# Kernel tuning notes

Measured on AMD Instinct MI355X. Metric: run time of the kernel, lower is better.

The kernel has to match this reference:

```python
import jax, jax.numpy as jnp
import numpy as np

D_MODEL = 1024
N_HEADS = 16
HEAD = D_MODEL // N_HEADS
SEQ_THRESHOLD = 2048
EPS = 1e-12  # torch F.normalize eps


def setup_inputs() -> dict:
    key = jax.random.key(0)
    ks = jax.random.split(key, 12)
    B, L = 2, 2048
    s = 1.0 / np.sqrt(D_MODEL)
    inp = {
        "query": jax.random.normal(ks[0], (B, L, D_MODEL), jnp.float32),
        "key": jax.random.normal(ks[1], (B, L, D_MODEL), jnp.float32),
        "value": jax.random.normal(ks[2], (B, L, D_MODEL), jnp.float32),
        "mask": jnp.ones((B, 1, 1, L), jnp.int32),
        "Wq": jax.random.normal(ks[3], (D_MODEL, D_MODEL), jnp.float32) * s,
        "bq": jnp.zeros((D_MODEL,), jnp.float32),
        "Wk": jax.random.normal(ks[4], (D_MODEL, D_MODEL), jnp.float32) * s,
        "bk": jnp.zeros((D_MODEL,), jnp.float32),
        "Wv": jax.random.normal(ks[5], (D_MODEL, D_MODEL), jnp.float32) * s,
        "bv": jnp.zeros((D_MODEL,), jnp.float32),
        "Wo": jax.random.normal(ks[6], (D_MODEL, D_MODEL), jnp.float32) * s,
        "bo": jnp.zeros((D_MODEL,), jnp.float32),
        "scale": jnp.asarray(np.log2(SEQ_THRESHOLD**2 - SEQ_THRESHOLD), jnp.float32),
    }
    return inp


def _split_heads(x):  # [B,L,D] -> [B,H,L,hd]
    B, L, _ = x.shape
    return x.reshape(B, L, N_HEADS, HEAD).transpose(0, 2, 1, 3)


def _l2norm(x):
    n = jnp.sqrt(jnp.sum(x * x, axis=-1, keepdims=True))
    return x / jnp.maximum(n, EPS)


def reference(query, key, value, mask, Wq, bq, Wk, bk, Wv, bv, Wo, bo, scale):
    Q = _split_heads(query @ Wq.T + bq)
    K = _split_heads(key @ Wk.T + bk)
    V = _split_heads(value @ Wv.T + bv)
    Q = _l2norm(Q)
    K = _l2norm(K)
    # scaled cosine attention scores [B,H,Lq,Lk]
    scores = scale * jnp.einsum("bhqd,bhkd->bhqk", Q, K)
    scores = jnp.where(mask == 0, jnp.float32(-1e18), scores)
    attn = jax.nn.softmax(scores, axis=-1)
    ctx = jnp.einsum("bhqk,bhkd->bhqd", attn, V)
    B, H, Lq, hd = ctx.shape
    ctx = ctx.transpose(0, 2, 1, 3).reshape(B, Lq, H * hd)
    out = ctx @ Wo.T + bo
    return (out, attn)
```

## Files before the change

### kernel.cpp

```cpp
#include <hip/hip_runtime.h>
#include <hip/hip_bf16.h>
#include <stdint.h>

typedef __attribute__((ext_vector_type(8))) short bf16x8;
typedef __attribute__((ext_vector_type(4))) float f32x4;

#define LSEQ 2048
#define DM 1024
#define NH 16
#define HD 64

__device__ __forceinline__ unsigned short bf16r(float f) {
  unsigned u = __builtin_bit_cast(unsigned, f);
  u = (u + 0x7FFFu + ((u >> 16) & 1u)) >> 16;
  return (unsigned short)u;
}
__device__ __forceinline__ float bf16f(unsigned short h) {
  unsigned u = ((unsigned)h) << 16;
  return __builtin_bit_cast(float, u);
}
__device__ __forceinline__ unsigned cvt_pk_bf16(float a, float b) {
  unsigned r;
  asm("v_cvt_pk_bf16_f32 %0, %1, %2" : "=v"(r) : "v"(a), "v"(b));
  return r;
}

__device__ __forceinline__ void async16(const void* g, void* l) {
  __builtin_amdgcn_global_load_lds(
      (const __attribute__((address_space(1))) unsigned int*)g,
      (__attribute__((address_space(3))) unsigned int*)l, 16, 0, 0);
}

__device__ __forceinline__ bf16x8 lds_frag_swz(const unsigned short* base, int row, int colbyte) {
  int addr = row * 128 + colbyte;
  addr ^= ((row & 7) << 4);
  return *(const bf16x8*)((const char*)base + addr);
}
__device__ __forceinline__ bf16x8 lds_frag_swzV(const unsigned short* base, int row, int colbyte) {
  int addr = row * 256 + colbyte;
  addr ^= ((row & 15) << 4);
  return *(const bf16x8*)((const char*)base + addr);
}

__global__ __launch_bounds__(256) void cvt3(const float* __restrict__ s0,
                                            const float* __restrict__ s1,
                                            const float* __restrict__ s2,
                                            unsigned short* __restrict__ d0,
                                            unsigned short* __restrict__ d1,
                                            unsigned short* __restrict__ d2, int n8) {
  int y = blockIdx.y;
  const float* s = (y == 0) ? s0 : (y == 1) ? s1 : s2;
  unsigned short* d = (y == 0) ? d0 : (y == 1) ? d1 : d2;
  int i = blockIdx.x * 256 + threadIdx.x;
  if (i >= n8) return;
  const float4* sp = (const float4*)s;
  float4 a = sp[2 * i], b = sp[2 * i + 1];
  union { unsigned short u[8]; uint4 v; } r;
  r.u[0] = bf16r(a.x); r.u[1] = bf16r(a.y); r.u[2] = bf16r(a.z); r.u[3] = bf16r(a.w);
  r.u[4] = bf16r(b.x); r.u[5] = bf16r(b.y); r.u[6] = bf16r(b.z); r.u[7] = bf16r(b.w);
  ((uint4*)d)[i] = r.v;
}
__global__ __launch_bounds__(256) void cvt4(const float* __restrict__ s0,
                                            const float* __restrict__ s1,
                                            const float* __restrict__ s2,
                                            const float* __restrict__ s3,
                                            unsigned short* __restrict__ d0,
                                            unsigned short* __restrict__ d1,
                                            unsigned short* __restrict__ d2,
                                            unsigned short* __restrict__ d3, int n8) {
  int y = blockIdx.y;
  const float* s = (y == 0) ? s0 : (y == 1) ? s1 : (y == 2) ? s2 : s3;
  unsigned short* d = (y == 0) ? d0 : (y == 1) ? d1 : (y == 2) ? d2 : d3;
  int i = blockIdx.x * 256 + threadIdx.x;
  if (i >= n8) return;
  const float4* sp = (const float4*)s;
  float4 a = sp[2 * i], b = sp[2 * i + 1];
  union { unsigned short u[8]; uint4 v; } r;
  r.u[0] = bf16r(a.x); r.u[1] = bf16r(a.y); r.u[2] = bf16r(a.z); r.u[3] = bf16r(a.w);
  r.u[4] = bf16r(b.x); r.u[5] = bf16r(b.y); r.u[6] = bf16r(b.z); r.u[7] = bf16r(b.w);
  ((uint4*)d)[i] = r.v;
}

template <int MODE>
__device__ __forceinline__ void gemm_core(const unsigned short* __restrict__ A,
                                          const unsigned short* __restrict__ Bw,
                                          const float* __restrict__ bias,
                                          void* __restrict__ Cout,
                                          unsigned short* As, unsigned short* Bs) {
  const int t = threadIdx.x, lane = t & 63, wid = t >> 6;
  const int mt = blockIdx.x, nt = blockIdx.y;
  const int wm = (wid >> 1) * 64, wn = (wid & 1) * 64;
  const int lq = lane >> 4, lr = lane & 15;

  f32x4 acc[4][4];
#pragma unroll
  for (int i = 0; i < 4; ++i)
#pragma unroll
    for (int j = 0; j < 4; ++j) acc[i][j] = (f32x4){0.f, 0.f, 0.f, 0.f};

  auto stage = [&](int k0) {
#pragma unroll
    for (int i = 0; i < 4; ++i) {
      int chunk = i * 256 + t;
      int row = chunk >> 3, j = chunk & 7;
      int sj = j ^ (row & 7);
      async16(A + (size_t)(mt * 128 + row) * DM + k0 + sj * 8, (char*)As + chunk * 16);
    }
#pragma unroll
    for (int i = 0; i < 4; ++i) {
      int chunk = i * 256 + t;
      int row = chunk >> 3, j = chunk & 7;
      int sj = j ^ (row & 7);
      async16(Bw + (size_t)(nt * 128 + row) * DM + k0 + sj * 8, (char*)Bs + chunk * 16);
    }
  };

  stage(0);
  for (int kt = 0; kt < DM / 64; ++kt) {
    __syncthreads();
    bf16x8 af[4][2], bfr[4][2];
#pragma unroll
    for (int mf = 0; mf < 4; ++mf) {
      int row = wm + mf * 16 + lr;
#pragma unroll
      for (int ks = 0; ks < 2; ++ks)
        af[mf][ks] = lds_frag_swz(As, row, ks * 64 + lq * 16);
    }
#pragma unroll
    for (int nf = 0; nf < 4; ++nf) {
      int row = wn + nf * 16 + lr;
#pragma unroll
      for (int ks = 0; ks < 2; ++ks)
        bfr[nf][ks] = lds_frag_swz(Bs, row, ks * 64 + lq * 16);
    }
    __syncthreads();
    if (kt + 1 < DM / 64) stage((kt + 1) * 64);
#pragma unroll
    for (int ks = 0; ks < 2; ++ks)
#pragma unroll
      for (int mf = 0; mf < 4; ++mf)
#pragma unroll
        for (int nf = 0; nf < 4; ++nf)
          acc[mf][nf] = __builtin_amdgcn_mfma_f32_16x16x32_bf16(af[mf][ks], bfr[nf][ks],
                                                                acc[mf][nf], 0, 0, 0);
  }

  const int gn0 = nt * 128 + wn;
  float bv[4];
#pragma unroll
  for (int nf = 0; nf < 4; ++nf) bv[nf] = bias[gn0 + nf * 16 + lr];
#pragma unroll
  for (int mf = 0; mf < 4; ++mf) {
    float v[4][4];
#pragma unroll
    for (int nf = 0; nf < 4; ++nf)
#pragma unroll
      for (int r = 0; r < 4; ++r) v[nf][r] = acc[mf][nf][r] + bv[nf];
    if (MODE == 1) {
#pragma unroll
      for (int r = 0; r < 4; ++r) {
        float ss = v[0][r] * v[0][r] + v[1][r] * v[1][r] + v[2][r] * v[2][r] + v[3][r] * v[3][r];
        ss += __shfl_xor(ss, 1, 64);
        ss += __shfl_xor(ss, 2, 64);
        ss += __shfl_xor(ss, 4, 64);
        ss += __shfl_xor(ss, 8, 64);
        float rn = 1.0f / fmaxf(sqrtf(ss), 1e-12f);
#pragma unroll
        for (int nf = 0; nf < 4; ++nf) v[nf][r] *= rn;
      }
    }
    const int gm0 = mt * 128 + wm + mf * 16 + lq * 4;
    if (MODE == 2) {
      float* C = (float*)Cout;
#pragma unroll
      for (int r = 0; r < 4; ++r)
#pragma unroll
        for (int nf = 0; nf < 4; ++nf)
          C[(size_t)(gm0 + r) * DM + gn0 + nf * 16 + lr] = v[nf][r];
    } else if (MODE == 3) {
      unsigned short* Vt = (unsigned short*)Cout;
      const int bb = gm0 >> 11, ll = gm0 & 2047;
#pragma unroll
      for (int nf = 0; nf < 4; ++nf) {
        int col = gn0 + nf * 16 + lr;
        int hh = col >> 6, dd = col & 63;
        ushort4 o;
        o.x = bf16r(v[nf][0]); o.y = bf16r(v[nf][1]);
        o.z = bf16r(v[nf][2]); o.w = bf16r(v[nf][3]);
        *(ushort4*)&Vt[(size_t)((bb * NH + hh) * HD + dd) * LSEQ + ll] = o;
      }
    } else {
      unsigned short* C = (unsigned short*)Cout;
#pragma unroll
      for (int r = 0; r < 4; ++r)
#pragma unroll
        for (int nf = 0; nf < 4; ++nf)
          C[(size_t)(gm0 + r) * DM + gn0 + nf * 16 + lr] = bf16r(v[nf][r]);
    }
  }
}

__global__ __launch_bounds__(256) void gemm_qkv(
    const unsigned short* __restrict__ A0, const unsigned short* __restrict__ A1,
    const unsigned short* __restrict__ A2, const unsigned short* __restrict__ W0,
    const unsigned short* __restrict__ W1, const unsigned short* __restrict__ W2,
    const float* __restrict__ b0, const float* __restrict__ b1, const float* __restrict__ b2,
    unsigned short* __restrict__ C0, unsigned short* __restrict__ C1,
    unsigned short* __restrict__ C2) {
  __shared__ unsigned short As[128 * 64];
  __shared__ unsigned short Bs[128 * 64];
  int z = blockIdx.z;
  if (z == 0) gemm_core<1>(A0, W0, b0, C0, As, Bs);
  else if (z == 1) gemm_core<1>(A1, W1, b1, C1, As, Bs);
  else gemm_core<3>(A2, W2, b2, C2, As, Bs);
}

__global__ __launch_bounds__(256) void gemm_o(const unsigned short* __restrict__ A,
                                              const unsigned short* __restrict__ W,
                                              const float* __restrict__ bias,
                                              float* __restrict__ C) {
  __shared__ unsigned short As[128 * 64];
  __shared__ unsigned short Bs[128 * 64];
  gemm_core<2>(A, W, bias, C, As, Bs);
}

__global__ __launch_bounds__(256, 4) void attn_kernel(
    const unsigned short* __restrict__ Qn, const unsigned short* __restrict__ Kn,
    const unsigned short* __restrict__ Vt, const int* __restrict__ mask,
    const float* __restrict__ scale_p, float* __restrict__ attn_out,
    unsigned short* __restrict__ ctx) {
  __shared__ unsigned short QVs[64 * 128];
  __shared__ unsigned short Ks[128 * 64];
  __shared__ unsigned short Ms[2048];
  const int qt = blockIdx.x, h = blockIdx.y, b = blockIdx.z;
  const int t = threadIdx.x, lane = t & 63, wid = t >> 6;
  const int lq = lane >> 4, lr = lane & 15;
  const int wq = wid * 16;
  const float k2 = scale_p[0] * 1.4426950408889634f;

  const unsigned short* Qg = Qn + ((size_t)(b * LSEQ + qt * 64) * DM + h * HD);
  const unsigned short* Kg = Kn + ((size_t)b * LSEQ * DM + h * HD);
  const unsigned short* Vg = Vt + (size_t)(b * NH + h) * HD * LSEQ;
  float* attn_g = attn_out + ((size_t)((b * NH + h) * LSEQ + qt * 64)) * LSEQ;
  const int* mg = mask + b * LSEQ;

  auto stageK = [&](int k0) {
#pragma unroll
    for (int i = 0; i < 4; ++i) {
      int chunk = i * 256 + t;
      int row = chunk >> 3, j = chunk & 7;
      async16(Kg + (size_t)(k0 + row) * DM + (j ^ (row & 7)) * 8, (char*)Ks + chunk * 16);
    }
  };
  auto stageV = [&](int k0) {
#pragma unroll
    for (int i = 0; i < 4; ++i) {
      int chunk = i * 256 + t;
      int row = chunk >> 4, j = chunk & 15;
      async16(Vg + (size_t)row * LSEQ + k0 + (j ^ (row & 15)) * 8, (char*)QVs + chunk * 16);
    }
  };

  {
    const int4* mp = (const int4*)mg;
    int4 m0 = mp[t * 2], m1 = mp[t * 2 + 1];
    union { unsigned short u[8]; uint4 v; } mo;
    mo.u[0] = m0.x ? 0x3F80 : 0; mo.u[1] = m0.y ? 0x3F80 : 0;
    mo.u[2] = m0.z ? 0x3F80 : 0; mo.u[3] = m0.w ? 0x3F80 : 0;
    mo.u[4] = m1.x ? 0x3F80 : 0; mo.u[5] = m1.y ? 0x3F80 : 0;
    mo.u[6] = m1.z ? 0x3F80 : 0; mo.u[7] = m1.w ? 0x3F80 : 0;
    ((uint4*)Ms)[t] = mo.v;
  }
#pragma unroll
  for (int i = 0; i < 2; ++i) {
    int chunk = i * 256 + t;
    int row = chunk >> 3, j = chunk & 7;
    async16(Qg + (size_t)row * DM + (j ^ (row & 7)) * 8, (char*)QVs + chunk * 16);
  }
  stageK(0);

  bf16x8 qa[2];
  float rsum = 0.f;

  for (int kt = 0; kt < LSEQ / 128; ++kt) {
    __syncthreads();
    if (kt == 0) {
      qa[0] = lds_frag_swz(QVs, wq + lr, lq * 16);
      qa[1] = lds_frag_swz(QVs, wq + lr, 64 + lq * 16);
    }
#pragma unroll
    for (int nf = 0; nf < 8; ++nf) {
      bf16x8 k0f = lds_frag_swz(Ks, nf * 16 + lr, lq * 16);
      bf16x8 k1f = lds_frag_swz(Ks, nf * 16 + lr, 64 + lq * 16);
      f32x4 z = (f32x4){0.f, 0.f, 0.f, 0.f};
      z = __builtin_amdgcn_mfma_f32_16x16x32_bf16(k0f, qa[0], z, 0, 0, 0);
      z = __builtin_amdgcn_mfma_f32_16x16x32_bf16(k1f, qa[1], z, 0, 0, 0);
      ushort4 m4 = *(const ushort4*)&Ms[kt * 128 + nf * 16 + lq * 4];
      rsum += exp2f(z[0] * k2) * bf16f(m4.x);
      rsum += exp2f(z[1] * k2) * bf16f(m4.y);
      rsum += exp2f(z[2] * k2) * bf16f(m4.z);
      rsum += exp2f(z[3] * k2) * bf16f(m4.w);
    }
    __syncthreads();
    if (kt + 1 < LSEQ / 128) stageK((kt + 1) * 128);
  }
  rsum += __shfl_xor(rsum, 16, 64);
  rsum += __shfl_xor(rsum, 32, 64);
  const float sinv = 1.0f / fmaxf(rsum, 1e-30f);

  stageK(0);
  stageV(0);
  f32x4 opv[4];
#pragma unroll
  for (int nf = 0; nf < 4; ++nf) opv[nf] = (f32x4){0.f, 0.f, 0.f, 0.f};
  const int s0 = (lq & 1) * 32 + lr, s1 = s0 + 16;
  const bool hi = (lq >> 1) != 0;

  for (int kt = 0; kt < LSEQ / 128; ++kt) {
    __syncthreads();
    unsigned pw[16];
#pragma unroll
    for (int nf = 0; nf < 8; ++nf) {
      bf16x8 k0f = lds_frag_swz(Ks, nf * 16 + lr, lq * 16);
      bf16x8 k1f = lds_frag_swz(Ks, nf * 16 + lr, 64 + lq * 16);
      f32x4 z = (f32x4){0.f, 0.f, 0.f, 0.f};
      z = __builtin_amdgcn_mfma_f32_16x16x32_bf16(k0f, qa[0], z, 0, 0, 0);
      z = __builtin_amdgcn_mfma_f32_16x16x32_bf16(k1f, qa[1], z, 0, 0, 0);
      ushort4 m4 = *(const ushort4*)&Ms[kt * 128 + nf * 16 + lq * 4];
      float p0 = exp2f(z[0] * k2) * bf16f(m4.x) * sinv;
      float p1 = exp2f(z[1] * k2) * bf16f(m4.y) * sinv;
      float p2 = exp2f(z[2] * k2) * bf16f(m4.z) * sinv;
      float p3 = exp2f(z[3] * k2) * bf16f(m4.w) * sinv;
      f32x4 st = (f32x4){p0, p1, p2, p3};
      __builtin_nontemporal_store(
          st, (f32x4*)(attn_g + (size_t)(wq + lr) * LSEQ + kt * 128 + nf * 16 + lq * 4));
      pw[nf * 2] = cvt_pk_bf16(p0, p1);
      pw[nf * 2 + 1] = cvt_pk_bf16(p2, p3);
    }
#pragma unroll
    for (int ks = 0; ks < 4; ++ks) {
      unsigned a0 = pw[4 * ks], a1 = pw[4 * ks + 1];
      unsigned b0 = pw[4 * ks + 2], b1 = pw[4 * ks + 3];
      unsigned ua0 = __shfl((int)a0, s0, 64), ua1 = __shfl((int)a1, s0, 64);
      unsigned ua2 = __shfl((int)a0, s1, 64), ua3 = __shfl((int)a1, s1, 64);
      unsigned ub0 = __shfl((int)b0, s0, 64), ub1 = __shfl((int)b1, s0, 64);
      unsigned ub2 = __shfl((int)b0, s1, 64), ub3 = __shfl((int)b1, s1, 64);
      union { unsigned w[4]; bf16x8 v; } pf;
      pf.w[0] = hi ? ub0 : ua0;
      pf.w[1] = hi ? ub1 : ua1;
      pf.w[2] = hi ? ub2 : ua2;
      pf.w[3] = hi ? ub3 : ua3;
#pragma unroll
      for (int nf = 0; nf < 4; ++nf) {
        bf16x8 vb = lds_frag_swzV(QVs, nf * 16 + lr, ks * 64 + lq * 16);
        opv[nf] = __builtin_amdgcn_mfma_f32_16x16x32_bf16(vb, pf.v, opv[nf], 0, 0, 0);
      }
    }
    __syncthreads();
    if (kt + 1 < LSEQ / 128) { stageK((kt + 1) * 128); stageV((kt + 1) * 128); }
  }
#pragma unroll
  for (int nf = 0; nf < 4; ++nf) {
    ushort4 o;
    o.x = bf16r(opv[nf][0]); o.y = bf16r(opv[nf][1]);
    o.z = bf16r(opv[nf][2]); o.w = bf16r(opv[nf][3]);
    *(ushort4*)&ctx[(size_t)(b * LSEQ + qt * 64 + wq + lr) * DM + h * HD + nf * 16 + lq * 4] = o;
  }
}

extern "C" void kernel_launch(void* const* d_in, const int* in_sizes, int n_in,
                              void* d_out, int out_size, void* d_ws, size_t ws_size,
                              hipStream_t stream) {
  const float* query = (const float*)d_in[0];
  const float* key_ = (const float*)d_in[1];
  const float* value = (const float*)d_in[2];
  const int* mask = (const int*)d_in[3];
  const float* Wq = (const float*)d_in[4];
  const float* bq = (const float*)d_in[5];
  const float* Wk = (const float*)d_in[6];
  const float* bk = (const float*)d_in[7];
  const float* Wv = (const float*)d_in[8];
  const float* bv = (const float*)d_in[9];
  const float* Wo = (const float*)d_in[10];
  const float* bo = (const float*)d_in[11];
  const float* scale = (const float*)d_in[12];

  char* ws = (char*)d_ws;
  const size_t XB = 8388608;
  const size_t WB = 2097152;
  unsigned short* qb = (unsigned short*)(ws);
  unsigned short* kb = (unsigned short*)(ws + XB);
  unsigned short* vb = (unsigned short*)(ws + 2 * XB);
  unsigned short* wqb = (unsigned short*)(ws + 3 * XB);
  unsigned short* wkb = (unsigned short*)(ws + 3 * XB + WB);
  unsigned short* wvb = (unsigned short*)(ws + 3 * XB + 2 * WB);
  unsigned short* wob = (unsigned short*)(ws + 3 * XB + 3 * WB);
  unsigned short* Qnb = (unsigned short*)(ws + 3 * XB + 4 * WB);
  unsigned short* Knb = (unsigned short*)(ws + 4 * XB + 4 * WB);
  unsigned short* Vtb = (unsigned short*)(ws + 5 * XB + 4 * WB);
  unsigned short* ctxb = (unsigned short*)(ws + 6 * XB + 4 * WB);

  cvt3<<<dim3(2048, 3), 256, 0, stream>>>(query, key_, value, qb, kb, vb, 524288);
  cvt4<<<dim3(512, 4), 256, 0, stream>>>(Wq, Wk, Wv, Wo, wqb, wkb, wvb, wob, 131072);

  gemm_qkv<<<dim3(32, 8, 3), 256, 0, stream>>>(qb, kb, vb, wqb, wkb, wvb, bq, bk, bv,
                                               Qnb, Knb, Vtb);

  float* attn_out = (float*)d_out + 4194304;
  attn_kernel<<<dim3(32, NH, 2), 256, 0, stream>>>(Qnb, Knb, Vtb, mask, scale, attn_out, ctxb);

  gemm_o<<<dim3(32, 8), 256, 0, stream>>>(ctxb, wob, bo, (float*)d_out);
}
```

Before: 287.9 us.

## Split attention warps 2x2 over query and key tiles, swizzle block order

Each warp now handles 32 query rows and half of each 128-key tile rather than 16 query rows and the full tile. Every K fragment loaded from LDS therefore feeds two query fragments, halving K fragment LDS reads per MFMA. Row sums and partial PV accumulators are combined across the two key-half warps through shared memory, which adds a sync and an LDS reduction at the end. The grid is flattened and swizzled so that consecutive blocks spread over heads and batches, and the exp2f calls become the hardware exp2 builtin.

```diff
diff --git a/kernel.cpp b/kernel.cpp
--- a/kernel.cpp
+++ b/kernel.cpp
@@ -232,10 +232,15 @@
   __shared__ unsigned short QVs[64 * 128];
   __shared__ unsigned short Ks[128 * 64];
   __shared__ unsigned short Ms[2048];
-  const int qt = blockIdx.x, h = blockIdx.y, b = blockIdx.z;
+  __shared__ float Rs[2][2][32];
+
+  const int raw = blockIdx.x;
+  const int swz = (raw & 7) * 128 + (raw >> 3);
+  const int qt = swz & 31, h = (swz >> 5) & 15, b = swz >> 9;
+
   const int t = threadIdx.x, lane = t & 63, wid = t >> 6;
   const int lq = lane >> 4, lr = lane & 15;
-  const int wq = wid * 16;
+  const int qg = wid >> 1, kg = wid & 1;
   const float k2 = scale_p[0] * 1.4426950408889634f;
 
   const unsigned short* Qg = Qn + ((size_t)(b * LSEQ + qt * 64) * DM + h * HD);
@@ -279,92 +284,152 @@
   }
   stageK(0);
 
-  bf16x8 qa[2];
-  float rsum = 0.f;
+  bf16x8 qb[2][2];
+  float rs[2] = {0.f, 0.f};
 
   for (int kt = 0; kt < LSEQ / 128; ++kt) {
     __syncthreads();
     if (kt == 0) {
-      qa[0] = lds_frag_swz(QVs, wq + lr, lq * 16);
-      qa[1] = lds_frag_swz(QVs, wq + lr, 64 + lq * 16);
-    }
-#pragma unroll
-    for (int nf = 0; nf < 8; ++nf) {
-      bf16x8 k0f = lds_frag_swz(Ks, nf * 16 + lr, lq * 16);
-      bf16x8 k1f = lds_frag_swz(Ks, nf * 16 + lr, 64 + lq * 16);
-      f32x4 z = (f32x4){0.f, 0.f, 0.f, 0.f};
-      z = __builtin_amdgcn_mfma_f32_16x16x32_bf16(k0f, qa[0], z, 0, 0, 0);
-      z = __builtin_amdgcn_mfma_f32_16x16x32_bf16(k1f, qa[1], z, 0, 0, 0);
-      ushort4 m4 = *(const ushort4*)&Ms[kt * 128 + nf * 16 + lq * 4];
-      rsum += exp2f(z[0] * k2) * bf16f(m4.x);
-      rsum += exp2f(z[1] * k2) * bf16f(m4.y);
-      rsum += exp2f(z[2] * k2) * bf16f(m4.z);
-      rsum += exp2f(z[3] * k2) * bf16f(m4.w);
+#pragma unroll
+      for (int qf = 0; qf < 2; ++qf)
+#pragma unroll
+        for (int dh = 0; dh < 2; ++dh)
+          qb[qf][dh] = lds_frag_swz(QVs, qg * 32 + qf * 16 + lr, dh * 64 + lq * 16);
+    }
+#pragma unroll
+    for (int kf = 0; kf < 4; ++kf) {
+      int krow = kg * 64 + kf * 16 + lr;
+      bf16x8 a0 = lds_frag_swz(Ks, krow, lq * 16);
+      bf16x8 a1 = lds_frag_swz(Ks, krow, 64 + lq * 16);
+      ushort4 m4 = *(const ushort4*)&Ms[kt * 128 + kg * 64 + kf * 16 + lq * 4];
+#pragma unroll
+      for (int qf = 0; qf < 2; ++qf) {
+        f32x4 z = (f32x4){0.f, 0.f, 0.f, 0.f};
+        z = __builtin_amdgcn_mfma_f32_16x16x32_bf16(a0, qb[qf][0], z, 0, 0, 0);
+        z = __builtin_amdgcn_mfma_f32_16x16x32_bf16(a1, qb[qf][1], z, 0, 0, 0);
+        rs[qf] += __builtin_amdgcn_exp2f(z[0] * k2) * bf16f(m4.x);
+        rs[qf] += __builtin_amdgcn_exp2f(z[1] * k2) * bf16f(m4.y);
+        rs[qf] += __builtin_amdgcn_exp2f(z[2] * k2) * bf16f(m4.z);
+        rs[qf] += __builtin_amdgcn_exp2f(z[3] * k2) * bf16f(m4.w);
+      }
     }
     __syncthreads();
     if (kt + 1 < LSEQ / 128) stageK((kt + 1) * 128);
   }
-  rsum += __shfl_xor(rsum, 16, 64);
-  rsum += __shfl_xor(rsum, 32, 64);
-  const float sinv = 1.0f / fmaxf(rsum, 1e-30f);
-
+#pragma unroll
+  for (int qf = 0; qf < 2; ++qf) {
+    rs[qf] += __shfl_xor(rs[qf], 16, 64);
+    rs[qf] += __shfl_xor(rs[qf], 32, 64);
+  }
+  if (lq == 0) {
+    Rs[qg][kg][lr] = rs[0];
+    Rs[qg][kg][16 + lr] = rs[1];
+  }
+  __syncthreads();
+  float sinv[2];
+#pragma unroll
+  for (int qf = 0; qf < 2; ++qf) {
+    float tot = Rs[qg][0][qf * 16 + lr] + Rs[qg][1][qf * 16 + lr];
+    sinv[qf] = 1.0f / fmaxf(tot, 1e-30f);
+  }
   stageK(0);
   stageV(0);
-  f32x4 opv[4];
-#pragma unroll
-  for (int nf = 0; nf < 4; ++nf) opv[nf] = (f32x4){0.f, 0.f, 0.f, 0.f};
-  const int s0 = (lq & 1) * 32 + lr, s1 = s0 + 16;
-  const bool hi = (lq >> 1) != 0;
+
+  f32x4 acc[4][2];
+#pragma unroll
+  for (int df = 0; df < 4; ++df)
+#pragma unroll
+    for (int qf = 0; qf < 2; ++qf) acc[df][qf] = (f32x4){0.f, 0.f, 0.f, 0.f};
+  const int sA = ((lane & 16) ? 32 : 0) + lr;
+  const int sB = sA + 16;
+  const bool selHi = (lane & 32) != 0;
 
   for (int kt = 0; kt < LSEQ / 128; ++kt) {
     __syncthreads();
-    unsigned pw[16];
-#pragma unroll
-    for (int nf = 0; nf < 8; ++nf) {
-      bf16x8 k0f = lds_frag_swz(Ks, nf * 16 + lr, lq * 16);
-      bf16x8 k1f = lds_frag_swz(Ks, nf * 16 + lr, 64 + lq * 16);
-      f32x4 z = (f32x4){0.f, 0.f, 0.f, 0.f};
-      z = __builtin_amdgcn_mfma_f32_16x16x32_bf16(k0f, qa[0], z, 0, 0, 0);
-      z = __builtin_amdgcn_mfma_f32_16x16x32_bf16(k1f, qa[1], z, 0, 0, 0);
-      ushort4 m4 = *(const ushort4*)&Ms[kt * 128 + nf * 16 + lq * 4];
-      float p0 = exp2f(z[0] * k2) * bf16f(m4.x) * sinv;
-      float p1 = exp2f(z[1] * k2) * bf16f(m4.y) * sinv;
-      float p2 = exp2f(z[2] * k2) * bf16f(m4.z) * sinv;
-      float p3 = exp2f(z[3] * k2) * bf16f(m4.w) * sinv;
-      f32x4 st = (f32x4){p0, p1, p2, p3};
-      __builtin_nontemporal_store(
-          st, (f32x4*)(attn_g + (size_t)(wq + lr) * LSEQ + kt * 128 + nf * 16 + lq * 4));
-      pw[nf * 2] = cvt_pk_bf16(p0, p1);
-      pw[nf * 2 + 1] = cvt_pk_bf16(p2, p3);
-    }
-#pragma unroll
-    for (int ks = 0; ks < 4; ++ks) {
-      unsigned a0 = pw[4 * ks], a1 = pw[4 * ks + 1];
-      unsigned b0 = pw[4 * ks + 2], b1 = pw[4 * ks + 3];
-      unsigned ua0 = __shfl((int)a0, s0, 64), ua1 = __shfl((int)a1, s0, 64);
-      unsigned ua2 = __shfl((int)a0, s1, 64), ua3 = __shfl((int)a1, s1, 64);
-      unsigned ub0 = __shfl((int)b0, s0, 64), ub1 = __shfl((int)b1, s0, 64);
-      unsigned ub2 = __shfl((int)b0, s1, 64), ub3 = __shfl((int)b1, s1, 64);
-      union { unsigned w[4]; bf16x8 v; } pf;
-      pf.w[0] = hi ? ub0 : ua0;
-      pf.w[1] = hi ? ub1 : ua1;
-      pf.w[2] = hi ? ub2 : ua2;
-      pf.w[3] = hi ? ub3 : ua3;
-#pragma unroll
-      for (int nf = 0; nf < 4; ++nf) {
-        bf16x8 vb = lds_frag_swzV(QVs, nf * 16 + lr, ks * 64 + lq * 16);
-        opv[nf] = __builtin_amdgcn_mfma_f32_16x16x32_bf16(vb, pf.v, opv[nf], 0, 0, 0);
+    unsigned pk[4][2][2];
+#pragma unroll
+    for (int kf = 0; kf < 4; ++kf) {
+      int krow = kg * 64 + kf * 16 + lr;
+      bf16x8 a0 = lds_frag_swz(Ks, krow, lq * 16);
+      bf16x8 a1 = lds_frag_swz(Ks, krow, 64 + lq * 16);
+      ushort4 m4 = *(const ushort4*)&Ms[kt * 128 + kg * 64 + kf * 16 + lq * 4];
+#pragma unroll
+      for (int qf = 0; qf < 2; ++qf) {
+        f32x4 z = (f32x4){0.f, 0.f, 0.f, 0.f};
+        z = __builtin_amdgcn_mfma_f32_16x16x32_bf16(a0, qb[qf][0], z, 0, 0, 0);
+        z = __builtin_amdgcn_mfma_f32_16x16x32_bf16(a1, qb[qf][1], z, 0, 0, 0);
+        float p0 = __builtin_amdgcn_exp2f(z[0] * k2) * bf16f(m4.x) * sinv[qf];
+        float p1 = __builtin_amdgcn_exp2f(z[1] * k2) * bf16f(m4.y) * sinv[qf];
+        float p2 = __builtin_amdgcn_exp2f(z[2] * k2) * bf16f(m4.z) * sinv[qf];
+        float p3 = __builtin_amdgcn_exp2f(z[3] * k2) * bf16f(m4.w) * sinv[qf];
+        f32x4 st = (f32x4){p0, p1, p2, p3};
+        __builtin_nontemporal_store(
+            st, (f32x4*)(attn_g + (size_t)(qg * 32 + qf * 16 + lr) * LSEQ + kt * 128 +
+                         kg * 64 + kf * 16 + lq * 4));
+        pk[kf][qf][0] = cvt_pk_bf16(p0, p1);
+        pk[kf][qf][1] = cvt_pk_bf16(p2, p3);
+      }
+    }
+#pragma unroll
+    for (int kh = 0; kh < 2; ++kh) {
+      bf16x8 pbv[2];
+#pragma unroll
+      for (int qf = 0; qf < 2; ++qf) {
+        union { unsigned w[4]; bf16x8 v; } pb;
+        unsigned lo0 = __shfl((int)pk[kh * 2][qf][0], sA, 64);
+        unsigned hi0 = __shfl((int)pk[kh * 2 + 1][qf][0], sA, 64);
+        unsigned lo1 = __shfl((int)pk[kh * 2][qf][1], sA, 64);
+        unsigned hi1 = __shfl((int)pk[kh * 2 + 1][qf][1], sA, 64);
+        unsigned lo2 = __shfl((int)pk[kh * 2][qf][0], sB, 64);
+        unsigned hi2 = __shfl((int)pk[kh * 2 + 1][qf][0], sB, 64);
+        unsigned lo3 = __shfl((int)pk[kh * 2][qf][1], sB, 64);
+        unsigned hi3 = __shfl((int)pk[kh * 2 + 1][qf][1], sB, 64);
+        pb.w[0] = selHi ? hi0 : lo0;
+        pb.w[1] = selHi ? hi1 : lo1;
+        pb.w[2] = selHi ? hi2 : lo2;
+        pb.w[3] = selHi ? hi3 : lo3;
+        pbv[qf] = pb.v;
+      }
+#pragma unroll
+      for (int df = 0; df < 4; ++df) {
+        bf16x8 va = lds_frag_swzV(QVs, df * 16 + lr, kg * 128 + kh * 64 + lq * 16);
+#pragma unroll
+        for (int qf = 0; qf < 2; ++qf)
+          acc[df][qf] = __builtin_amdgcn_mfma_f32_16x16x32_bf16(va, pbv[qf], acc[df][qf], 0, 0, 0);
       }
     }
     __syncthreads();
     if (kt + 1 < LSEQ / 128) { stageK((kt + 1) * 128); stageV((kt + 1) * 128); }
   }
-#pragma unroll
-  for (int nf = 0; nf < 4; ++nf) {
-    ushort4 o;
-    o.x = bf16r(opv[nf][0]); o.y = bf16r(opv[nf][1]);
-    o.z = bf16r(opv[nf][2]); o.w = bf16r(opv[nf][3]);
-    *(ushort4*)&ctx[(size_t)(b * LSEQ + qt * 64 + wq + lr) * DM + h * HD + nf * 16 + lq * 4] = o;
+
+  __syncthreads();
+  float* CR = (float*)Ks;
+  if (kg == 1) {
+#pragma unroll
+    for (int df = 0; df < 4; ++df)
+#pragma unroll
+      for (int qf = 0; qf < 2; ++qf) {
+        int q = qf * 16 + lr, dd = df * 16 + lq * 4;
+        int byte = ((qg * 32 + q) * 64 + dd) * 4;
+        byte ^= (q & 7) << 4;
+        *(f32x4*)((char*)CR + byte) = acc[df][qf];
+      }
+  }
+  __syncthreads();
+  if (kg == 0) {
+#pragma unroll
+    for (int df = 0; df < 4; ++df)
+#pragma unroll
+      for (int qf = 0; qf < 2; ++qf) {
+        int q = qf * 16 + lr, dd = df * 16 + lq * 4;
+        int byte = ((qg * 32 + q) * 64 + dd) * 4;
+        byte ^= (q & 7) << 4;
+        f32x4 o = *(const f32x4*)((const char*)CR + byte);
+        o += acc[df][qf];
+        ushort4 st;
+        st.x = bf16r(o[0]); st.y = bf16r(o[1]); st.z = bf16r(o[2]); st.w = bf16r(o[3]);
+        *(ushort4*)&ctx[(size_t)(b * LSEQ + qt * 64 + qg * 32 + q) * DM + h * HD + dd] = st;
+      }
   }
 }
 
@@ -407,7 +472,7 @@
                                                Qnb, Knb, Vtb);
 
   float* attn_out = (float*)d_out + 4194304;
-  attn_kernel<<<dim3(32, NH, 2), 256, 0, stream>>>(Qnb, Knb, Vtb, mask, scale, attn_out, ctxb);
+  attn_kernel<<<1024, 256, 0, stream>>>(Qnb, Knb, Vtb, mask, scale, attn_out, ctxb);
 
   gemm_o<<<dim3(32, 8), 256, 0, stream>>>(ctxb, wob, bo, (float*)d_out);
 }
```

Result: faster. 268.7 us (-6.7%).

## Load attention K/V fragments directly from global memory and swizzle block order

Applied to the files above, without the earlier changes.

The attention kernel stops staging Q, K and V tiles through LDS with async copies and barriers. Each wave now reads its MFMA fragments straight from global memory and relies on L2/cache reuse across waves. The grid is flattened and remapped so that blocks sharing a head and batch run close together in time. The kernel also switches to the raw exp2 intrinsic. This drops LDS traffic and the syncthreads, but each wave fetches K/V redundantly with strided 16-byte global loads, so latency may become exposed.

```diff
diff --git a/kernel.cpp b/kernel.cpp
--- a/kernel.cpp
+++ b/kernel.cpp
@@ -34,11 +34,6 @@
 __device__ __forceinline__ bf16x8 lds_frag_swz(const unsigned short* base, int row, int colbyte) {
   int addr = row * 128 + colbyte;
   addr ^= ((row & 7) << 4);
-  return *(const bf16x8*)((const char*)base + addr);
-}
-__device__ __forceinline__ bf16x8 lds_frag_swzV(const unsigned short* base, int row, int colbyte) {
-  int addr = row * 256 + colbyte;
-  addr ^= ((row & 15) << 4);
   return *(const bf16x8*)((const char*)base + addr);
 }
 
@@ -229,13 +224,14 @@
     const unsigned short* __restrict__ Vt, const int* __restrict__ mask,
     const float* __restrict__ scale_p, float* __restrict__ attn_out,
     unsigned short* __restrict__ ctx) {
-  __shared__ unsigned short QVs[64 * 128];
-  __shared__ unsigned short Ks[128 * 64];
   __shared__ unsigned short Ms[2048];
-  const int qt = blockIdx.x, h = blockIdx.y, b = blockIdx.z;
+
+  const int raw = blockIdx.x;
+  const int swz = (raw & 7) * 128 + (raw >> 3);
+  const int qt = swz & 31, h = (swz >> 5) & 15, b = swz >> 9;
+
   const int t = threadIdx.x, lane = t & 63, wid = t >> 6;
   const int lq = lane >> 4, lr = lane & 15;
-  const int wq = wid * 16;
   const float k2 = scale_p[0] * 1.4426950408889634f;
 
   const unsigned short* Qg = Qn + ((size_t)(b * LSEQ + qt * 64) * DM + h * HD);
@@ -243,23 +239,6 @@
   const unsigned short* Vg = Vt + (size_t)(b * NH + h) * HD * LSEQ;
   float* attn_g = attn_out + ((size_t)((b * NH + h) * LSEQ + qt * 64)) * LSEQ;
   const int* mg = mask + b * LSEQ;
-
-  auto stageK = [&](int k0) {
-#pragma unroll
-    for (int i = 0; i < 4; ++i) {
-      int chunk = i * 256 + t;
-      int row = chunk >> 3, j = chunk & 7;
-      async16(Kg + (size_t)(k0 + row) * DM + (j ^ (row & 7)) * 8, (char*)Ks + chunk * 16);
-    }
-  };
-  auto stageV = [&](int k0) {
-#pragma unroll
-    for (int i = 0; i < 4; ++i) {
-      int chunk = i * 256 + t;
-      int row = chunk >> 4, j = chunk & 15;
-      async16(Vg + (size_t)row * LSEQ + k0 + (j ^ (row & 15)) * 8, (char*)QVs + chunk * 16);
-    }
-  };
 
   {
     const int4* mp = (const int4*)mg;
@@ -271,100 +250,97 @@
     mo.u[6] = m1.z ? 0x3F80 : 0; mo.u[7] = m1.w ? 0x3F80 : 0;
     ((uint4*)Ms)[t] = mo.v;
   }
-#pragma unroll
-  for (int i = 0; i < 2; ++i) {
-    int chunk = i * 256 + t;
-    int row = chunk >> 3, j = chunk & 7;
-    async16(Qg + (size_t)row * DM + (j ^ (row & 7)) * 8, (char*)QVs + chunk * 16);
-  }
-  stageK(0);
-
-  bf16x8 qa[2];
-  float rsum = 0.f;
-
+  bf16x8 qb[2];
+  {
+    const unsigned short* qp = Qg + (size_t)(wid * 16 + lr) * DM + lq * 8;
+    qb[0] = *(const bf16x8*)qp;
+    qb[1] = *(const bf16x8*)(qp + 32);
+  }
+  __syncthreads();
+
+  float rs = 0.f;
+#pragma unroll 1
   for (int kt = 0; kt < LSEQ / 128; ++kt) {
-    __syncthreads();
-    if (kt == 0) {
-      qa[0] = lds_frag_swz(QVs, wq + lr, lq * 16);
-      qa[1] = lds_frag_swz(QVs, wq + lr, 64 + lq * 16);
-    }
-#pragma unroll
-    for (int nf = 0; nf < 8; ++nf) {
-      bf16x8 k0f = lds_frag_swz(Ks, nf * 16 + lr, lq * 16);
-      bf16x8 k1f = lds_frag_swz(Ks, nf * 16 + lr, 64 + lq * 16);
+    const unsigned short* kbase = Kg + (size_t)(kt * 128 + lr) * DM + lq * 8;
+#pragma unroll
+    for (int kf = 0; kf < 8; ++kf) {
+      const unsigned short* kp = kbase + kf * 16 * DM;
+      bf16x8 a0 = *(const bf16x8*)kp;
+      bf16x8 a1 = *(const bf16x8*)(kp + 32);
       f32x4 z = (f32x4){0.f, 0.f, 0.f, 0.f};
-      z = __builtin_amdgcn_mfma_f32_16x16x32_bf16(k0f, qa[0], z, 0, 0, 0);
-      z = __builtin_amdgcn_mfma_f32_16x16x32_bf16(k1f, qa[1], z, 0, 0, 0);
-      ushort4 m4 = *(const ushort4*)&Ms[kt * 128 + nf * 16 + lq * 4];
-      rsum += exp2f(z[0] * k2) * bf16f(m4.x);
-      rsum += exp2f(z[1] * k2) * bf16f(m4.y);
-      rsum += exp2f(z[2] * k2) * bf16f(m4.z);
-      rsum += exp2f(z[3] * k2) * bf16f(m4.w);
-    }
-    __syncthreads();
-    if (kt + 1 < LSEQ / 128) stageK((kt + 1) * 128);
-  }
-  rsum += __shfl_xor(rsum, 16, 64);
-  rsum += __shfl_xor(rsum, 32, 64);
-  const float sinv = 1.0f / fmaxf(rsum, 1e-30f);
-
-  stageK(0);
-  stageV(0);
-  f32x4 opv[4];
-#pragma unroll
-  for (int nf = 0; nf < 4; ++nf) opv[nf] = (f32x4){0.f, 0.f, 0.f, 0.f};
-  const int s0 = (lq & 1) * 32 + lr, s1 = s0 + 16;
-  const bool hi = (lq >> 1) != 0;
-
+      z = __builtin_amdgcn_mfma_f32_16x16x32_bf16(a0, qb[0], z, 0, 0, 0);
+      z = __builtin_amdgcn_mfma_f32_16x16x32_bf16(a1, qb[1], z, 0, 0, 0);
+      ushort4 m4 = *(const ushort4*)&Ms[kt * 128 + kf * 16 + lq * 4];
+      rs += __builtin_amdgcn_exp2f(z[0] * k2) * bf16f(m4.x);
+      rs += __builtin_amdgcn_exp2f(z[1] * k2) * bf16f(m4.y);
+      rs += __builtin_amdgcn_exp2f(z[2] * k2) * bf16f(m4.z);
+      rs += __builtin_amdgcn_exp2f(z[3] * k2) * bf16f(m4.w);
+    }
+  }
+  rs += __shfl_xor(rs, 16, 64);
+  rs += __shfl_xor(rs, 32, 64);
+  const float sinv = 1.0f / fmaxf(rs, 1e-30f);
+
+  f32x4 acc[4];
+#pragma unroll
+  for (int df = 0; df < 4; ++df) acc[df] = (f32x4){0.f, 0.f, 0.f, 0.f};
+  const int sA = ((lane & 16) ? 32 : 0) + lr;
+  const int sB = sA + 16;
+  const bool selHi = (lane & 32) != 0;
+
+#pragma unroll 1
   for (int kt = 0; kt < LSEQ / 128; ++kt) {
-    __syncthreads();
-    unsigned pw[16];
-#pragma unroll
-    for (int nf = 0; nf < 8; ++nf) {
-      bf16x8 k0f = lds_frag_swz(Ks, nf * 16 + lr, lq * 16);
-      bf16x8 k1f = lds_frag_swz(Ks, nf * 16 + lr, 64 + lq * 16);
+    unsigned pk[8][2];
+    const unsigned short* kbase = Kg + (size_t)(kt * 128 + lr) * DM + lq * 8;
+#pragma unroll
+    for (int kf = 0; kf < 8; ++kf) {
+      const unsigned short* kp = kbase + kf * 16 * DM;
+      bf16x8 a0 = *(const bf16x8*)kp;
+      bf16x8 a1 = *(const bf16x8*)(kp + 32);
       f32x4 z = (f32x4){0.f, 0.f, 0.f, 0.f};
-      z = __builtin_amdgcn_mfma_f32_16x16x32_bf16(k0f, qa[0], z, 0, 0, 0);
-      z = __builtin_amdgcn_mfma_f32_16x16x32_bf16(k1f, qa[1], z, 0, 0, 0);
-      ushort4 m4 = *(const ushort4*)&Ms[kt * 128 + nf * 16 + lq * 4];
-      float p0 = exp2f(z[0] * k2) * bf16f(m4.x) * sinv;
-      float p1 = exp2f(z[1] * k2) * bf16f(m4.y) * sinv;
-      float p2 = exp2f(z[2] * k2) * bf16f(m4.z) * sinv;
-      float p3 = exp2f(z[3] * k2) * bf16f(m4.w) * sinv;
+      z = __builtin_amdgcn_mfma_f32_16x16x32_bf16(a0, qb[0], z, 0, 0, 0);
+      z = __builtin_amdgcn_mfma_f32_16x16x32_bf16(a1, qb[1], z, 0, 0, 0);
+      ushort4 m4 = *(const ushort4*)&Ms[kt * 128 + kf * 16 + lq * 4];
+      float p0 = __builtin_amdgcn_exp2f(z[0] * k2) * bf16f(m4.x) * sinv;
+      float p1 = __builtin_amdgcn_exp2f(z[1] * k2) * bf16f(m4.y) * sinv;
+      float p2 = __builtin_amdgcn_exp2f(z[2] * k2) * bf16f(m4.z) * sinv;
+      float p3 = __builtin_amdgcn_exp2f(z[3] * k2) * bf16f(m4.w) * sinv;
       f32x4 st = (f32x4){p0, p1, p2, p3};
       __builtin_nontemporal_store(
-          st, (f32x4*)(attn_g + (size_t)(wq + lr) * LSEQ + kt * 128 + nf * 16 + lq * 4));
-      pw[nf * 2] = cvt_pk_bf16(p0, p1);
-      pw[nf * 2 + 1] = cvt_pk_bf16(p2, p3);
-    }
-#pragma unroll
-    for (int ks = 0; ks < 4; ++ks) {
-      unsigned a0 = pw[4 * ks], a1 = pw[4 * ks + 1];
-      unsigned b0 = pw[4 * ks + 2], b1 = pw[4 * ks + 3];
-      unsigned ua0 = __shfl((int)a0, s0, 64), ua1 = __shfl((int)a1, s0, 64);
-      unsigned ua2 = __shfl((int)a0, s1, 64), ua3 = __shfl((int)a1, s1, 64);
-      unsigned ub0 = __shfl((int)b0, s0, 64), ub1 = __shfl((int)b1, s0, 64);
-      unsigned ub2 = __shfl((int)b0, s1, 64), ub3 = __shfl((int)b1, s1, 64);
-      union { unsigned w[4]; bf16x8 v; } pf;
-      pf.w[0] = hi ? ub0 : ua0;
-      pf.w[1] = hi ? ub1 : ua1;
-      pf.w[2] = hi ? ub2 : ua2;
-      pf.w[3] = hi ? ub3 : ua3;
-#pragma unroll
-      for (int nf = 0; nf < 4; ++nf) {
-        bf16x8 vb = lds_frag_swzV(QVs, nf * 16 + lr, ks * 64 + lq * 16);
-        opv[nf] = __builtin_amdgcn_mfma_f32_16x16x32_bf16(vb, pf.v, opv[nf], 0, 0, 0);
+          st, (f32x4*)(attn_g + (size_t)(wid * 16 + lr) * LSEQ + kt * 128 + kf * 16 + lq * 4));
+      pk[kf][0] = cvt_pk_bf16(p0, p1);
+      pk[kf][1] = cvt_pk_bf16(p2, p3);
+    }
+#pragma unroll
+    for (int kh = 0; kh < 4; ++kh) {
+      union { unsigned w[4]; bf16x8 v; } pb;
+      unsigned lo0 = __shfl((int)pk[kh * 2][0], sA, 64);
+      unsigned hi0 = __shfl((int)pk[kh * 2 + 1][0], sA, 64);
+      unsigned lo1 = __shfl((int)pk[kh * 2][1], sA, 64);
+      unsigned hi1 = __shfl((int)pk[kh * 2 + 1][1], sA, 64);
+      unsigned lo2 = __shfl((int)pk[kh * 2][0], sB, 64);
+      unsigned hi2 = __shfl((int)pk[kh * 2 + 1][0], sB, 64);
+      unsigned lo3 = __shfl((int)pk[kh * 2][1], sB, 64);
+      unsigned hi3 = __shfl((int)pk[kh * 2 + 1][1], sB, 64);
+      pb.w[0] = selHi ? hi0 : lo0;
+      pb.w[1] = selHi ? hi1 : lo1;
+      pb.w[2] = selHi ? hi2 : lo2;
+      pb.w[3] = selHi ? hi3 : lo3;
+      const unsigned short* vbase = Vg + (size_t)lr * LSEQ + kt * 128 + kh * 32 + lq * 8;
+#pragma unroll
+      for (int df = 0; df < 4; ++df) {
+        bf16x8 va = *(const bf16x8*)(vbase + (size_t)df * 16 * LSEQ);
+        acc[df] = __builtin_amdgcn_mfma_f32_16x16x32_bf16(va, pb.v, acc[df], 0, 0, 0);
       }
     }
-    __syncthreads();
-    if (kt + 1 < LSEQ / 128) { stageK((kt + 1) * 128); stageV((kt + 1) * 128); }
-  }
-#pragma unroll
-  for (int nf = 0; nf < 4; ++nf) {
+  }
+#pragma unroll
+  for (int df = 0; df < 4; ++df) {
     ushort4 o;
-    o.x = bf16r(opv[nf][0]); o.y = bf16r(opv[nf][1]);
-    o.z = bf16r(opv[nf][2]); o.w = bf16r(opv[nf][3]);
-    *(ushort4*)&ctx[(size_t)(b * LSEQ + qt * 64 + wq + lr) * DM + h * HD + nf * 16 + lq * 4] = o;
+    o.x = bf16r(acc[df][0]); o.y = bf16r(acc[df][1]);
+    o.z = bf16r(acc[df][2]); o.w = bf16r(acc[df][3]);
+    *(ushort4*)&ctx[(size_t)(b * LSEQ + qt * 64 + wid * 16 + lr) * DM + h * HD + df * 16 +
+                    lq * 4] = o;
   }
 }
 
@@ -407,7 +383,7 @@
                                                Qnb, Knb, Vtb);
 
   float* attn_out = (float*)d_out + 4194304;
-  attn_kernel<<<dim3(32, NH, 2), 256, 0, stream>>>(Qnb, Knb, Vtb, mask, scale, attn_out, ctxb);
+  attn_kernel<<<1024, 256, 0, stream>>>(Qnb, Knb, Vtb, mask, scale, attn_out, ctxb);
 
   gemm_o<<<dim3(32, 8), 256, 0, stream>>>(ctxb, wob, bo, (float*)d_out);
 }
```

Measured after the change: 441.4 us. 53.3% more time.
